# Optimization experiments

Measured on AMD Instinct MI355X. Metric: run time of the kernel, lower is better.

The kernel has to match this reference:

```python
import jax, jax.numpy as jnp
import numpy as np

P = 2          # patch size
DEPTH = 3
NHEAD = 8
DROP_RATIO = 0.15
LN_EPS = 1e-5


def _ln(x, g, b):
    m = jnp.mean(x, axis=-1, keepdims=True)
    v = jnp.mean((x - m) ** 2, axis=-1, keepdims=True)
    return (x - m) * jax.lax.rsqrt(v + LN_EPS) * g + b


def setup_inputs() -> dict:
    key = jax.random.key(0)
    ks = jax.random.split(key, 16)
    B, C, HW, D, L = 4, 3, 96, 256, DEPTH
    N = (HW // P) ** 2
    s = 0.02
    return {
        "x": jax.random.normal(ks[0], (B, C, HW, HW), jnp.float32),
        "patch_w": jax.random.normal(ks[1], (D, C, P, P), jnp.float32) * s,
        "patch_b": jnp.zeros((D,), jnp.float32),
        "pos": jax.random.normal(ks[2], (1, N, D), jnp.float32) * s,
        "imp_w1": jax.random.normal(ks[3], (D, 256), jnp.float32) * s,
        "imp_b1": jnp.zeros((256,), jnp.float32),
        "imp_w2": jax.random.normal(ks[4], (256, 1), jnp.float32) * s,
        "imp_b2": jnp.zeros((1,), jnp.float32),
        "ln1_g": jnp.ones((L, D), jnp.float32),
        "ln1_b": jnp.zeros((L, D), jnp.float32),
        "qkv_w": jax.random.normal(ks[5], (L, D, 3 * D), jnp.float32) * s,
        "qkv_b": jnp.zeros((L, 3 * D), jnp.float32),
        "proj_w": jax.random.normal(ks[6], (L, D, D), jnp.float32) * s,
        "proj_b": jnp.zeros((L, D), jnp.float32),
        "ln2_g": jnp.ones((L, D), jnp.float32),
        "ln2_b": jnp.zeros((L, D), jnp.float32),
        "mlp_w1": jax.random.normal(ks[7], (L, D, 4 * D), jnp.float32) * s,
        "mlp_b1": jnp.zeros((L, 4 * D), jnp.float32),
        "mlp_w2": jax.random.normal(ks[8], (L, 4 * D, D), jnp.float32) * s,
        "mlp_b2": jnp.zeros((L, D), jnp.float32),
        "out_g": jnp.ones((D,), jnp.float32),
        "out_b": jnp.zeros((D,), jnp.float32),
    }


def reference(x, patch_w, patch_b, pos, imp_w1, imp_b1, imp_w2, imp_b2,
              ln1_g, ln1_b, qkv_w, qkv_b, proj_w, proj_b,
              ln2_g, ln2_b, mlp_w1, mlp_b1, mlp_w2, mlp_b2, out_g, out_b):
    B, C, H, W = x.shape
    D = patch_w.shape[0]
    Hc, Wc = H // P, W // P
    # Patch embed: conv(k=stride=P) == blocked einsum  -> (B, N, D)
    xr = x.reshape(B, C, Hc, P, Wc, P)
    tokens = jnp.einsum('bchpwq,dcpq->bhwd', xr, patch_w).reshape(B, Hc * Wc, D) + patch_b
    tokens = tokens + pos
    B, N, _ = tokens.shape

    # Importance scores -> bottom-k keys masked (Eq.8-10)
    h = jax.nn.relu(tokens @ imp_w1 + imp_b1)
    scores = jax.nn.sigmoid((h @ imp_w2 + imp_b2)[..., 0])  # (B, N)
    k = int(DROP_RATIO * N)
    _, idx = jax.lax.top_k(-scores, k)                      # k smallest scores
    md = jnp.zeros((B, N), bool).at[jnp.arange(B)[:, None], idx].set(True)

    dk = D // NHEAD
    scale = 1.0 / np.sqrt(dk)
    for l in range(DEPTH):
        hln = _ln(tokens, ln1_g[l], ln1_b[l])
        qkv = hln @ qkv_w[l] + qkv_b[l]
        q, kk, v = jnp.split(qkv, 3, axis=-1)
        q = q.reshape(B, N, NHEAD, dk).transpose(0, 2, 1, 3)
        kk = kk.reshape(B, N, NHEAD, dk).transpose(0, 2, 1, 3)
        v = v.reshape(B, N, NHEAD, dk).transpose(0, 2, 1, 3)
        logits = jnp.einsum('bhnd,bhmd->bhnm', q, kk) * scale
        logits = jnp.where(md[:, None, None, :], -jnp.inf, logits)
        attn = jax.nn.softmax(logits, axis=-1)
        out = jnp.einsum('bhnm,bhmd->bhnd', attn, v)
        out = out.transpose(0, 2, 1, 3).reshape(B, N, D)
        tokens = tokens + (out @ proj_w[l] + proj_b[l])
        h2 = _ln(tokens, ln2_g[l], ln2_b[l])
        tokens = tokens + (jax.nn.gelu(h2 @ mlp_w1[l] + mlp_b1[l], approximate=False) @ mlp_w2[l] + mlp_b2[l])

    tokens = _ln(tokens, out_g, out_b)
    return tokens.mean(axis=1)  # (B, D)
```

## Files before the change

### kernel.cpp

```cpp
#include <hip/hip_runtime.h>
#include <hip/hip_bf16.h>
#include <math.h>

#define BATCH 4
#define NTOK  2304
#define DIM   256
#define NHEADS 8
#define HCDIM 48
#define KSEL  345
#define NKEEP 1959
#define NKC   1984
#define KT    31
#define KREM  39
#define LN_EPS 1e-5f

typedef unsigned short u16;
typedef __attribute__((ext_vector_type(8))) short bf16x8;
typedef __attribute__((ext_vector_type(4))) float f32x4;

__device__ __forceinline__ u16 f2bf(float x) {
  union { float f; unsigned u; } v; v.f = x;
  return (u16)((v.u + 0x7FFFu + ((v.u >> 16) & 1u)) >> 16);
}

__device__ __forceinline__ void gload_lds16(const u16* g, u16* l) {
  __builtin_amdgcn_global_load_lds((const __attribute__((address_space(1))) void*)g,
                                   (__attribute__((address_space(3))) void*)l, 16, 0, 0);
}

__global__ __launch_bounds__(256) void k_patch_embed(
    const float* __restrict__ x, const float* __restrict__ pw,
    const float* __restrict__ pb, const float* __restrict__ pos,
    float* __restrict__ tokens) {
  int blk = blockIdx.x;
  int b = blk / NTOK, n = blk % NTOK;
  int hc = n / HCDIM, wc = n % HCDIM;
  __shared__ float xs[12];
  int t = threadIdx.x;
  if (t < 12) {
    int c = t >> 2, p = (t >> 1) & 1, q = t & 1;
    xs[t] = x[((b * 3 + c) * 96 + (hc * 2 + p)) * 96 + (wc * 2 + q)];
  }
  __syncthreads();
  float acc = pb[t];
#pragma unroll
  for (int i = 0; i < 12; ++i) acc += xs[i] * pw[t * 12 + i];
  tokens[(size_t)(b * NTOK + n) * DIM + t] = acc + pos[n * DIM + t];
}

__global__ __launch_bounds__(256) void k_importance(
    const float* __restrict__ tokens, const float* __restrict__ w1,
    const float* __restrict__ b1, const float* __restrict__ w2,
    const float* __restrict__ b2, float* __restrict__ scores) {
  __shared__ float ts[16 * 256];
  __shared__ float hw[16 * 256];
  int base = blockIdx.x * 16;
  int t = threadIdx.x;
  for (int i = t; i < 16 * 256; i += 256) ts[i] = tokens[(size_t)base * 256 + i];
  __syncthreads();
  float acc[16];
#pragma unroll
  for (int r = 0; r < 16; ++r) acc[r] = b1[t];
  for (int i = 0; i < 256; ++i) {
    float w = w1[i * 256 + t];
#pragma unroll
    for (int r = 0; r < 16; ++r) acc[r] += ts[r * 256 + i] * w;
  }
  float w2v = w2[t];
#pragma unroll
  for (int r = 0; r < 16; ++r) hw[r * 256 + t] = fmaxf(acc[r], 0.f) * w2v;
  __syncthreads();
  if (t < 16) {
    float s = b2[0];
    for (int i = 0; i < 256; ++i) s += hw[t * 256 + i];
    scores[base + t] = 1.f / (1.f + expf(-s));
  }
}

__global__ __launch_bounds__(256) void k_select(const float* __restrict__ scores,
                                                int* __restrict__ cmap,
                                                u16* __restrict__ kvc) {
  int b = blockIdx.x, t = threadIdx.x;
  __shared__ unsigned sb[NTOK];
  __shared__ int cnt;
  __shared__ int pfl[256], pfe[256];
  __shared__ int remS;
  for (int i = t; i < NTOK; i += 256) sb[i] = __float_as_uint(scores[b * NTOK + i]);
  __syncthreads();
  unsigned prefix = 0;
  int r = KSEL;
  for (int bit = 31; bit >= 0; --bit) {
    if (t == 0) cnt = 0;
    __syncthreads();
    unsigned bmask = 1u << bit;
    unsigned hmask = (bit == 31) ? 0u : ~((bmask << 1) - 1u);
    int local = 0;
    for (int i = t; i < NTOK; i += 256)
      if ((sb[i] & hmask) == prefix && !(sb[i] & bmask)) local++;
    if (local) atomicAdd(&cnt, local);
    __syncthreads();
    int c0 = cnt;
    if (r > c0) { r -= c0; prefix |= bmask; }
    __syncthreads();
  }
  unsigned v = prefix;
  int cl = 0, ce = 0;
  int j0 = t * 9;
  for (int j = j0; j < j0 + 9; ++j) { cl += (sb[j] < v); ce += (sb[j] == v); }
  pfl[t] = cl; pfe[t] = ce;
  __syncthreads();
  if (t == 0) {
    int pl = 0, pe = 0;
    for (int i = 0; i < 256; ++i) {
      int a = pfl[i], e = pfe[i];
      pfl[i] = pl; pfe[i] = pe;
      pl += a; pe += e;
    }
    remS = KSEL - pl;
  }
  __syncthreads();
  int pl = pfl[t], pe = pfe[t], rem = remS;
  for (int j = j0; j < j0 + 9; ++j) {
    bool less = sb[j] < v, eq = sb[j] == v;
    bool drop = less || (eq && pe < rem);
    int dropped_before = pl + (pe < rem ? pe : rem);
    cmap[b * NTOK + j] = drop ? -1 : (j - dropped_before);
    pl += less; pe += eq;
  }
  for (int i = t; i < (NKC - NKEEP) * 512; i += 256)
    kvc[((size_t)b * NKC + NKEEP) * 512 + i] = 0;
}

__global__ __launch_bounds__(256) void k_ln4bf(
    const float* __restrict__ in, u16* __restrict__ out,
    const float* __restrict__ g, const float* __restrict__ bta) {
  int w = threadIdx.x >> 6, l = threadIdx.x & 63;
  size_t row = (size_t)blockIdx.x * 4 + w;
  float4 v = *(const float4*)(in + row * DIM + l * 4);
  float s = v.x + v.y + v.z + v.w;
  float ss = v.x * v.x + v.y * v.y + v.z * v.z + v.w * v.w;
#pragma unroll
  for (int o = 1; o < 64; o <<= 1) { s += __shfl_xor(s, o); ss += __shfl_xor(ss, o); }
  float m = s * (1.f / DIM);
  float inv = rsqrtf(ss * (1.f / DIM) - m * m + LN_EPS);
  float4 gv = *(const float4*)(g + l * 4);
  float4 bv = *(const float4*)(bta + l * 4);
  union { ushort4 u4; __hip_bfloat162 h2[2]; } o4;
  o4.h2[0] = __float22bfloat162_rn(make_float2((v.x - m) * inv * gv.x + bv.x,
                                               (v.y - m) * inv * gv.y + bv.y));
  o4.h2[1] = __float22bfloat162_rn(make_float2((v.z - m) * inv * gv.z + bv.z,
                                               (v.w - m) * inv * gv.w + bv.w));
  *(ushort4*)(out + row * DIM + l * 4) = o4.u4;
}

__global__ __launch_bounds__(256) void k_lnmean(
    const float* __restrict__ in, const float* __restrict__ g,
    const float* __restrict__ bta, float* __restrict__ part) {
  int chunk = blockIdx.x, b = blockIdx.y;
  int w = threadIdx.x >> 6, l = threadIdx.x & 63;
  float4 gv = *(const float4*)(g + l * 4);
  float4 bv = *(const float4*)(bta + l * 4);
  float4 acc = make_float4(0.f, 0.f, 0.f, 0.f);
  for (int i = 0; i < 16; ++i) {
    size_t row = (size_t)b * NTOK + chunk * 64 + w * 16 + i;
    float4 v = *(const float4*)(in + row * DIM + l * 4);
    float s = v.x + v.y + v.z + v.w;
    float ss = v.x * v.x + v.y * v.y + v.z * v.z + v.w * v.w;
#pragma unroll
    for (int o = 1; o < 64; o <<= 1) { s += __shfl_xor(s, o); ss += __shfl_xor(ss, o); }
    float m = s * (1.f / DIM);
    float inv = rsqrtf(ss * (1.f / DIM) - m * m + LN_EPS);
    acc.x += (v.x - m) * inv * gv.x + bv.x;
    acc.y += (v.y - m) * inv * gv.y + bv.y;
    acc.z += (v.z - m) * inv * gv.z + bv.z;
    acc.w += (v.w - m) * inv * gv.w + bv.w;
  }
  __shared__ float4 red[4][64];
  red[w][l] = acc;
  __syncthreads();
  if (w == 0) {
    float4 a0 = red[0][l], a1 = red[1][l], a2 = red[2][l], a3 = red[3][l];
    float4 tot = make_float4(a0.x + a1.x + a2.x + a3.x, a0.y + a1.y + a2.y + a3.y,
                             a0.z + a1.z + a2.z + a3.z, a0.w + a1.w + a2.w + a3.w);
    *(float4*)(part + ((size_t)b * 36 + chunk) * DIM + l * 4) = tot;
  }
}

__global__ __launch_bounds__(256) void k_mean_final(const float* __restrict__ part,
                                                    float* __restrict__ out) {
  int b = blockIdx.x, d = threadIdx.x;
  float s = 0.f;
  for (int c = 0; c < 36; ++c) s += part[(size_t)(b * 36 + c) * DIM + d];
  out[b * DIM + d] = s * (1.0f / NTOK);
}

__global__ __launch_bounds__(256) void k_wtrans_all(
    const float* __restrict__ qkv_w, const float* __restrict__ proj_w,
    const float* __restrict__ mlp_w1, const float* __restrict__ mlp_w2,
    u16* __restrict__ wq, u16* __restrict__ wp,
    u16* __restrict__ w1, u16* __restrict__ w2) {
  int id = blockIdx.x;
  const float* W; u16* WT; int K, N, m;
  if (id < 576)       { m = id;        K = 256;  N = 768;  W = qkv_w;  WT = wq; }
  else if (id < 768)  { m = id - 576;  K = 256;  N = 256;  W = proj_w; WT = wp; }
  else if (id < 1536) { m = id - 768;  K = 256;  N = 1024; W = mlp_w1; WT = w1; }
  else                { m = id - 1536; K = 1024; N = 256;  W = mlp_w2; WT = w2; }
  int ntiles = N / 32, tilesPerLayer = ntiles * (K / 32);
  int layer = m / tilesPerLayer, tid = m % tilesPerLayer;
  int nb = (tid % ntiles) * 32, kb = (tid / ntiles) * 32;
  const float* Wl = W + (size_t)layer * K * N;
  u16* WTl = WT + (size_t)layer * K * N;
  __shared__ float tile[32][33];
  int tx = threadIdx.x & 31, ty = threadIdx.x >> 5;
  for (int i = 0; i < 32; i += 8) tile[ty + i][tx] = Wl[(size_t)(kb + ty + i) * N + nb + tx];
  __syncthreads();
  for (int i = 0; i < 32; i += 8)
    WTl[(size_t)(nb + ty + i) * K + kb + tx] = f2bf(tile[tx][ty + i]);
}

__global__ __launch_bounds__(256) void k_gemm_bf16(
    const u16* __restrict__ A, const u16* __restrict__ BT,
    const float* __restrict__ bias, u16* __restrict__ outb,
    int K, int N, int act) {
  __shared__ __align__(16) u16 As[2][128 * 32];
  __shared__ __align__(16) u16 Bs[2][128 * 32];
  int t = threadIdx.x;
  int m0 = blockIdx.y * 128, n0 = blockIdx.x * 128;
  int w = t >> 6, l = t & 63, lr = l & 15, qd = l >> 4;
  int wm = (w >> 1) * 64, wn = (w & 1) * 64;
  const u16* gA = A + (size_t)(m0 + w * 16 + (l >> 2)) * K + (l & 3) * 8;
  const u16* gA2 = gA + (size_t)64 * K;
  const u16* gB = BT + (size_t)(n0 + w * 16 + (l >> 2)) * K + (l & 3) * 8;
  const u16* gB2 = gB + (size_t)64 * K;
  f32x4 acc[4][4];
#pragma unroll
  for (int i = 0; i < 4; ++i)
#pragma unroll
    for (int j = 0; j < 4; ++j)
#pragma unroll
      for (int r = 0; r < 4; ++r) acc[i][j][r] = 0.f;
  gload_lds16(gA, As[0] + w * 512);
  gload_lds16(gA2, As[0] + 2048 + w * 512);
  gload_lds16(gB, Bs[0] + w * 512);
  gload_lds16(gB2, Bs[0] + 2048 + w * 512);
  int nchunks = K >> 5;
  for (int c = 0; c < nchunks; ++c) {
    int buf = c & 1;
    __syncthreads();
    if (c + 1 < nchunks) {
      int k0 = (c + 1) << 5;
      gload_lds16(gA + k0, As[buf ^ 1] + w * 512);
      gload_lds16(gA2 + k0, As[buf ^ 1] + 2048 + w * 512);
      gload_lds16(gB + k0, Bs[buf ^ 1] + w * 512);
      gload_lds16(gB2 + k0, Bs[buf ^ 1] + 2048 + w * 512);
    }
    bf16x8 af[4], bfr[4];
#pragma unroll
    for (int mt = 0; mt < 4; ++mt)
      af[mt] = *(const bf16x8*)(As[buf] + (wm + mt * 16 + lr) * 32 + qd * 8);
#pragma unroll
    for (int nt = 0; nt < 4; ++nt)
      bfr[nt] = *(const bf16x8*)(Bs[buf] + (wn + nt * 16 + lr) * 32 + qd * 8);
#pragma unroll
    for (int mt = 0; mt < 4; ++mt)
#pragma unroll
      for (int nt = 0; nt < 4; ++nt)
        acc[mt][nt] = __builtin_amdgcn_mfma_f32_16x16x32_bf16(af[mt], bfr[nt],
                                                              acc[mt][nt], 0, 0, 0);
  }
#pragma unroll
  for (int mt = 0; mt < 4; ++mt) {
#pragma unroll
    for (int nt = 0; nt < 4; ++nt) {
#pragma unroll
      for (int r = 0; r < 4; ++r) {
        size_t m = (size_t)m0 + wm + mt * 16 + qd * 4 + r;
        int c = n0 + wn + nt * 16 + lr;
        float val = acc[mt][nt][r] + bias[c];
        if (act) val = 0.5f * val * (1.f + erff(val * 0.70710678118654752f));
        outb[m * N + c] = f2bf(val);
      }
    }
  }
}

__global__ __launch_bounds__(256) void k_gemm_qkv(
    const u16* __restrict__ A, const u16* __restrict__ BT,
    const float* __restrict__ bias, const int* __restrict__ cmap,
    u16* __restrict__ Qb, u16* __restrict__ KVc) {
  const int K = 256, N = 768;
  __shared__ __align__(16) u16 As[2][128 * 32];
  __shared__ __align__(16) u16 Bs[2][128 * 32];
  int t = threadIdx.x;
  int m0 = blockIdx.y * 128, n0 = blockIdx.x * 128;
  int w = t >> 6, l = t & 63, lr = l & 15, qd = l >> 4;
  int wm = (w >> 1) * 64, wn = (w & 1) * 64;
  const u16* gA = A + (size_t)(m0 + w * 16 + (l >> 2)) * K + (l & 3) * 8;
  const u16* gA2 = gA + (size_t)64 * K;
  const u16* gB = BT + (size_t)(n0 + w * 16 + (l >> 2)) * K + (l & 3) * 8;
  const u16* gB2 = gB + (size_t)64 * K;
  f32x4 acc[4][4];
#pragma unroll
  for (int i = 0; i < 4; ++i)
#pragma unroll
    for (int j = 0; j < 4; ++j)
#pragma unroll
      for (int r = 0; r < 4; ++r) acc[i][j][r] = 0.f;
  gload_lds16(gA, As[0] + w * 512);
  gload_lds16(gA2, As[0] + 2048 + w * 512);
  gload_lds16(gB, Bs[0] + w * 512);
  gload_lds16(gB2, Bs[0] + 2048 + w * 512);
  for (int c = 0; c < 8; ++c) {
    int buf = c & 1;
    __syncthreads();
    if (c + 1 < 8) {
      int k0 = (c + 1) << 5;
      gload_lds16(gA + k0, As[buf ^ 1] + w * 512);
      gload_lds16(gA2 + k0, As[buf ^ 1] + 2048 + w * 512);
      gload_lds16(gB + k0, Bs[buf ^ 1] + w * 512);
      gload_lds16(gB2 + k0, Bs[buf ^ 1] + 2048 + w * 512);
    }
    bf16x8 af[4], bfr[4];
#pragma unroll
    for (int mt = 0; mt < 4; ++mt)
      af[mt] = *(const bf16x8*)(As[buf] + (wm + mt * 16 + lr) * 32 + qd * 8);
#pragma unroll
    for (int nt = 0; nt < 4; ++nt)
      bfr[nt] = *(const bf16x8*)(Bs[buf] + (wn + nt * 16 + lr) * 32 + qd * 8);
#pragma unroll
    for (int mt = 0; mt < 4; ++mt)
#pragma unroll
      for (int nt = 0; nt < 4; ++nt)
        acc[mt][nt] = __builtin_amdgcn_mfma_f32_16x16x32_bf16(af[mt], bfr[nt],
                                                              acc[mt][nt], 0, 0, 0);
  }
  bool isQ = (n0 + wn) < 256;
#pragma unroll
  for (int mt = 0; mt < 4; ++mt) {
#pragma unroll
    for (int r = 0; r < 4; ++r) {
      int m = m0 + wm + mt * 16 + qd * 4 + r;
      int cpos = isQ ? 0 : cmap[m];
      int b = m / NTOK;
#pragma unroll
      for (int nt = 0; nt < 4; ++nt) {
        int c = n0 + wn + nt * 16 + lr;
        float val = acc[mt][nt][r] + bias[c];
        if (isQ) {
          Qb[(size_t)m * 256 + c] = f2bf(val * 0.17677669529663687f);
        } else if (cpos >= 0) {
          KVc[((size_t)b * NKC + cpos) * 512 + (c - 256)] = f2bf(val);
        }
      }
    }
  }
}

__global__ __launch_bounds__(256) void k_gemm_n64(
    const u16* __restrict__ A, const u16* __restrict__ BT,
    const float* __restrict__ bias, const float* __restrict__ res,
    float* __restrict__ outf, int K, int N) {
  __shared__ __align__(16) u16 As[2][128 * 32];
  __shared__ __align__(16) u16 Bs[2][64 * 32];
  int t = threadIdx.x;
  int m0 = blockIdx.y * 128, n0 = blockIdx.x * 64;
  int w = t >> 6, l = t & 63, lr = l & 15, qd = l >> 4;
  int wm = (w >> 1) * 64, wn = (w & 1) * 32;
  const u16* gA = A + (size_t)(m0 + w * 16 + (l >> 2)) * K + (l & 3) * 8;
  const u16* gA2 = gA + (size_t)64 * K;
  const u16* gB = BT + (size_t)(n0 + w * 16 + (l >> 2)) * K + (l & 3) * 8;
  f32x4 acc[4][2];
#pragma unroll
  for (int i = 0; i < 4; ++i)
#pragma unroll
    for (int j = 0; j < 2; ++j)
#pragma unroll
      for (int r = 0; r < 4; ++r) acc[i][j][r] = 0.f;
  gload_lds16(gA, As[0] + w * 512);
  gload_lds16(gA2, As[0] + 2048 + w * 512);
  gload_lds16(gB, Bs[0] + w * 512);
  int nchunks = K >> 5;
  for (int c = 0; c < nchunks; ++c) {
    int buf = c & 1;
    __syncthreads();
    if (c + 1 < nchunks) {
      int k0 = (c + 1) << 5;
      gload_lds16(gA + k0, As[buf ^ 1] + w * 512);
      gload_lds16(gA2 + k0, As[buf ^ 1] + 2048 + w * 512);
      gload_lds16(gB + k0, Bs[buf ^ 1] + w * 512);
    }
    bf16x8 af[4], bfr[2];
#pragma unroll
    for (int mt = 0; mt < 4; ++mt)
      af[mt] = *(const bf16x8*)(As[buf] + (wm + mt * 16 + lr) * 32 + qd * 8);
#pragma unroll
    for (int nt = 0; nt < 2; ++nt)
      bfr[nt] = *(const bf16x8*)(Bs[buf] + (wn + nt * 16 + lr) * 32 + qd * 8);
#pragma unroll
    for (int mt = 0; mt < 4; ++mt)
#pragma unroll
      for (int nt = 0; nt < 2; ++nt)
        acc[mt][nt] = __builtin_amdgcn_mfma_f32_16x16x32_bf16(af[mt], bfr[nt],
                                                              acc[mt][nt], 0, 0, 0);
  }
#pragma unroll
  for (int mt = 0; mt < 4; ++mt) {
#pragma unroll
    for (int nt = 0; nt < 2; ++nt) {
#pragma unroll
      for (int r = 0; r < 4; ++r) {
        size_t m = (size_t)m0 + wm + mt * 16 + qd * 4 + r;
        int c = n0 + wn + nt * 16 + lr;
        outf[m * N + c] = acc[mt][nt][r] + bias[c] + res[m * N + c];
      }
    }
  }
}

__global__ __launch_bounds__(256) void k_attn4(
    const u16* __restrict__ Qb, const u16* __restrict__ KVc,
    u16* __restrict__ outb) {
  int qt = blockIdx.x, h = blockIdx.y, b = blockIdx.z;
  int t = threadIdx.x, w = t >> 6, l = t & 63, lr = l & 15, qd = l >> 4;
  __shared__ __align__(16) u16 Ks[2][64 * 32];
  __shared__ __align__(16) u16 Vt[2][32][80];
  __shared__ __align__(16) u16 Pq[4][32][80];
  const short ONE = (short)0x3F80;
  int q0 = qt * 128 + w * 32;
  const u16* kvb = KVc + (size_t)b * NKC * 512;
  bf16x8 qf[2];
  qf[0] = *(const bf16x8*)(Qb + ((size_t)(b * NTOK) + q0 + lr) * 256 + h * 32 + qd * 8);
  qf[1] = *(const bf16x8*)(Qb + ((size_t)(b * NTOK) + q0 + 16 + lr) * 256 + h * 32 + qd * 8);
  const u16* gK = kvb + (size_t)(t >> 2) * 512 + h * 32 + (t & 3) * 8;
  const u16* gV = kvb + (size_t)l * 512 + 256 + h * 32 + w * 8;
  gload_lds16(gK, &Ks[0][w * 512]);
  bf16x8 vr = *(const bf16x8*)(gV);
  f32x4 oa[2][2];
  f32x4 lacc[2];
#pragma unroll
  for (int r = 0; r < 4; ++r) {
    oa[0][0][r] = 0.f; oa[0][1][r] = 0.f; oa[1][0][r] = 0.f; oa[1][1][r] = 0.f;
    lacc[0][r] = 0.f; lacc[1][r] = 0.f;
  }
  bf16x8 ones;
#pragma unroll
  for (int j = 0; j < 8; ++j) ones[j] = ONE;
  for (int kt = 0; kt < KT; ++kt) {
    int buf = kt & 1;
#pragma unroll
    for (int j = 0; j < 8; ++j) Vt[buf][w * 8 + j][l] = (u16)vr[j];
    __syncthreads();
    if (kt + 1 < KT) {
      size_t off = (size_t)(kt + 1) * 64 * 512;
      gload_lds16(gK + off, &Ks[buf ^ 1][w * 512]);
      vr = *(const bf16x8*)(gV + off);
    }
    bf16x8 kf[4];
#pragma unroll
    for (int nt = 0; nt < 4; ++nt)
      kf[nt] = *(const bf16x8*)(&Ks[buf][(nt * 16 + lr) * 32 + qd * 8]);
#pragma unroll
    for (int qh = 0; qh < 2; ++qh) {
      f32x4 p4[4];
#pragma unroll
      for (int nt = 0; nt < 4; ++nt) {
        f32x4 z; z[0] = 0.f; z[1] = 0.f; z[2] = 0.f; z[3] = 0.f;
        p4[nt] = __builtin_amdgcn_mfma_f32_16x16x32_bf16(kf[nt], qf[qh], z, 0, 0, 0);
      }
#pragma unroll
      for (int nt = 0; nt < 4; ++nt)
#pragma unroll
        for (int r = 0; r < 4; ++r) p4[nt][r] = __expf(p4[nt][r]);
#pragma unroll
      for (int nt = 0; nt < 4; ++nt) {
        union { ushort4 u4; __hip_bfloat162 h2[2]; } pu;
        pu.h2[0] = __float22bfloat162_rn(make_float2(p4[nt][0], p4[nt][1]));
        pu.h2[1] = __float22bfloat162_rn(make_float2(p4[nt][2], p4[nt][3]));
        *(ushort4*)(&Pq[w][qh * 16 + lr][nt * 16 + qd * 4]) = pu.u4;
      }
    }
    bf16x8 of1 = ones;
    if (kt == KT - 1) {
#pragma unroll
      for (int j = 0; j < 8; ++j) of1[j] = (32 + qd * 8 + j < KREM) ? ONE : (short)0;
    }
#pragma unroll
    for (int qh = 0; qh < 2; ++qh) {
#pragma unroll
      for (int kh = 0; kh < 2; ++kh) {
        bf16x8 pf = *(const bf16x8*)(&Pq[w][qh * 16 + lr][kh * 32 + qd * 8]);
#pragma unroll
        for (int dh = 0; dh < 2; ++dh) {
          bf16x8 vf = *(const bf16x8*)(&Vt[buf][dh * 16 + lr][kh * 32 + qd * 8]);
          oa[qh][dh] = __builtin_amdgcn_mfma_f32_16x16x32_bf16(pf, vf, oa[qh][dh], 0, 0, 0);
        }
        lacc[qh] = __builtin_amdgcn_mfma_f32_16x16x32_bf16(
            pf, kh ? of1 : ones, lacc[qh], 0, 0, 0);
      }
    }
  }
#pragma unroll
  for (int qh = 0; qh < 2; ++qh) {
#pragma unroll
    for (int r = 0; r < 4; ++r) {
      float inv = 1.f / lacc[qh][r];
      size_t row = (size_t)b * NTOK + q0 + qh * 16 + qd * 4 + r;
      outb[row * 256 + h * 32 + lr] = f2bf(oa[qh][0][r] * inv);
      outb[row * 256 + h * 32 + 16 + lr] = f2bf(oa[qh][1][r] * inv);
    }
  }
}

extern "C" void kernel_launch(void* const* d_in, const int* in_sizes, int n_in,
                              void* d_out, int out_size, void* d_ws, size_t ws_size,
                              hipStream_t stream) {
  (void)in_sizes; (void)n_in; (void)out_size;
  const float* x       = (const float*)d_in[0];
  const float* patch_w = (const float*)d_in[1];
  const float* patch_b = (const float*)d_in[2];
  const float* pos     = (const float*)d_in[3];
  const float* imp_w1  = (const float*)d_in[4];
  const float* imp_b1  = (const float*)d_in[5];
  const float* imp_w2  = (const float*)d_in[6];
  const float* imp_b2  = (const float*)d_in[7];
  const float* ln1_g   = (const float*)d_in[8];
  const float* ln1_b   = (const float*)d_in[9];
  const float* qkv_w   = (const float*)d_in[10];
  const float* qkv_b   = (const float*)d_in[11];
  const float* proj_w  = (const float*)d_in[12];
  const float* proj_b  = (const float*)d_in[13];
  const float* ln2_g   = (const float*)d_in[14];
  const float* ln2_b   = (const float*)d_in[15];
  const float* mlp_w1  = (const float*)d_in[16];
  const float* mlp_b1  = (const float*)d_in[17];
  const float* mlp_w2  = (const float*)d_in[18];
  const float* mlp_b2  = (const float*)d_in[19];
  const float* out_g   = (const float*)d_in[20];
  const float* out_b   = (const float*)d_in[21];
  float* out = (float*)d_out;

  const int M = BATCH * NTOK;
  const size_t TOK = (size_t)M * DIM;

  char* p = (char*)d_ws;
  float* tokens = (float*)p;       p += TOK * 4;
  float* scoresp = (float*)p;      p += (size_t)M * 4;
  int* cmap = (int*)p;             p += (size_t)M * 4;
  u16* act_bf = (u16*)p;           p += TOK * 2;
  u16* Qb = (u16*)p;               p += TOK * 2;
  u16* kvc = (u16*)p;              p += (size_t)BATCH * NKC * 512 * 2;
  u16* big_bf = (u16*)p;           p += (size_t)M * 1024 * 2;
  u16* wq_t = (u16*)p;             p += (size_t)3 * 768 * 256 * 2;
  u16* wp_t = (u16*)p;             p += (size_t)3 * 256 * 256 * 2;
  u16* w1_t = (u16*)p;             p += (size_t)3 * 1024 * 256 * 2;
  u16* w2_t = (u16*)p;             p += (size_t)3 * 256 * 1024 * 2;
  float* partials = (float*)act_bf;
  if (ws_size < (size_t)(p - (char*)d_ws)) return;

  k_wtrans_all<<<dim3(2304), 256, 0, stream>>>(qkv_w, proj_w, mlp_w1, mlp_w2,
                                               wq_t, wp_t, w1_t, w2_t);
  k_patch_embed<<<dim3(M), 256, 0, stream>>>(x, patch_w, patch_b, pos, tokens);
  k_importance<<<dim3(M / 16), 256, 0, stream>>>(tokens, imp_w1, imp_b1, imp_w2, imp_b2, scoresp);
  k_select<<<dim3(BATCH), 256, 0, stream>>>(scoresp, cmap, kvc);

  for (int l = 0; l < 3; ++l) {
    k_ln4bf<<<dim3(M / 4), 256, 0, stream>>>(tokens, act_bf, ln1_g + l * DIM, ln1_b + l * DIM);
    k_gemm_qkv<<<dim3(6, 72), 256, 0, stream>>>(
        act_bf, wq_t + (size_t)l * 768 * 256, qkv_b + l * 768, cmap, Qb, kvc);
    k_attn4<<<dim3(18, NHEADS, BATCH), 256, 0, stream>>>(Qb, kvc, act_bf);
    k_gemm_n64<<<dim3(4, 72), 256, 0, stream>>>(
        act_bf, wp_t + (size_t)l * 256 * 256, proj_b + l * DIM, tokens, tokens, 256, 256);
    k_ln4bf<<<dim3(M / 4), 256, 0, stream>>>(tokens, act_bf, ln2_g + l * DIM, ln2_b + l * DIM);
    k_gemm_bf16<<<dim3(8, 72), 256, 0, stream>>>(
        act_bf, w1_t + (size_t)l * 1024 * 256, mlp_b1 + l * 1024, big_bf, 256, 1024, 1);
    k_gemm_n64<<<dim3(4, 72), 256, 0, stream>>>(
        big_bf, w2_t + (size_t)l * 256 * 1024, mlp_b2 + l * DIM, tokens, tokens, 1024, 256);
  }
  k_lnmean<<<dim3(36, BATCH), 256, 0, stream>>>(tokens, out_g, out_b, partials);
  k_mean_final<<<dim3(BATCH), 256, 0, stream>>>(partials, out);
}
```

Baseline: 613.6 us.

## Swizzle LDS tiles, shrink attention and N64 GEMM tiles, use exp2 softmax

Applies an XOR swizzle to the LDS column offsets in all GEMM kernels and the attention K tile, aiming to cut LDS bank conflicts on the bf16x8 fragment reads. Halves the M tile of the N=256 GEMM (64x64 tiles, twice as many blocks) and halves the query rows per wave in attention (16 instead of 32, twice as many blocks), trading per-block reuse for more parallelism across CUs. Folds log2(e) into the Q scale so the softmax can use a native exp2 instead of __expf. The smaller attention tiles reload K/V more often, and the smaller GEMM tiles reload more weight data.

```diff
diff --git a/kernel.cpp b/kernel.cpp
--- a/kernel.cpp
+++ b/kernel.cpp
@@ -13,6 +13,7 @@
 #define KT    31
 #define KREM  39
 #define LN_EPS 1e-5f
+#define QSCALE 0.25508688726880056f
 
 typedef unsigned short u16;
 typedef __attribute__((ext_vector_type(8))) short bf16x8;
@@ -228,9 +229,11 @@
   int m0 = blockIdx.y * 128, n0 = blockIdx.x * 128;
   int w = t >> 6, l = t & 63, lr = l & 15, qd = l >> 4;
   int wm = (w >> 1) * 64, wn = (w & 1) * 64;
-  const u16* gA = A + (size_t)(m0 + w * 16 + (l >> 2)) * K + (l & 3) * 8;
+  int sc = ((t & 3) ^ ((t >> 4) & 3)) * 8;
+  int rc = (qd ^ ((lr >> 2) & 3)) * 8;
+  const u16* gA = A + (size_t)(m0 + w * 16 + (l >> 2)) * K + sc;
   const u16* gA2 = gA + (size_t)64 * K;
-  const u16* gB = BT + (size_t)(n0 + w * 16 + (l >> 2)) * K + (l & 3) * 8;
+  const u16* gB = BT + (size_t)(n0 + w * 16 + (l >> 2)) * K + sc;
   const u16* gB2 = gB + (size_t)64 * K;
   f32x4 acc[4][4];
 #pragma unroll
@@ -257,10 +260,10 @@
     bf16x8 af[4], bfr[4];
 #pragma unroll
     for (int mt = 0; mt < 4; ++mt)
-      af[mt] = *(const bf16x8*)(As[buf] + (wm + mt * 16 + lr) * 32 + qd * 8);
+      af[mt] = *(const bf16x8*)(As[buf] + (wm + mt * 16 + lr) * 32 + rc);
 #pragma unroll
     for (int nt = 0; nt < 4; ++nt)
-      bfr[nt] = *(const bf16x8*)(Bs[buf] + (wn + nt * 16 + lr) * 32 + qd * 8);
+      bfr[nt] = *(const bf16x8*)(Bs[buf] + (wn + nt * 16 + lr) * 32 + rc);
 #pragma unroll
     for (int mt = 0; mt < 4; ++mt)
 #pragma unroll
@@ -295,9 +298,11 @@
   int m0 = blockIdx.y * 128, n0 = blockIdx.x * 128;
   int w = t >> 6, l = t & 63, lr = l & 15, qd = l >> 4;
   int wm = (w >> 1) * 64, wn = (w & 1) * 64;
-  const u16* gA = A + (size_t)(m0 + w * 16 + (l >> 2)) * K + (l & 3) * 8;
+  int sc = ((t & 3) ^ ((t >> 4) & 3)) * 8;
+  int rc = (qd ^ ((lr >> 2) & 3)) * 8;
+  const u16* gA = A + (size_t)(m0 + w * 16 + (l >> 2)) * K + sc;
   const u16* gA2 = gA + (size_t)64 * K;
-  const u16* gB = BT + (size_t)(n0 + w * 16 + (l >> 2)) * K + (l & 3) * 8;
+  const u16* gB = BT + (size_t)(n0 + w * 16 + (l >> 2)) * K + sc;
   const u16* gB2 = gB + (size_t)64 * K;
   f32x4 acc[4][4];
 #pragma unroll
@@ -323,10 +328,10 @@
     bf16x8 af[4], bfr[4];
 #pragma unroll
     for (int mt = 0; mt < 4; ++mt)
-      af[mt] = *(const bf16x8*)(As[buf] + (wm + mt * 16 + lr) * 32 + qd * 8);
+      af[mt] = *(const bf16x8*)(As[buf] + (wm + mt * 16 + lr) * 32 + rc);
 #pragma unroll
     for (int nt = 0; nt < 4; ++nt)
-      bfr[nt] = *(const bf16x8*)(Bs[buf] + (wn + nt * 16 + lr) * 32 + qd * 8);
+      bfr[nt] = *(const bf16x8*)(Bs[buf] + (wn + nt * 16 + lr) * 32 + rc);
 #pragma unroll
     for (int mt = 0; mt < 4; ++mt)
 #pragma unroll
@@ -347,7 +352,7 @@
         int c = n0 + wn + nt * 16 + lr;
         float val = acc[mt][nt][r] + bias[c];
         if (isQ) {
-          Qb[(size_t)m * 256 + c] = f2bf(val * 0.17677669529663687f);
+          Qb[(size_t)m * 256 + c] = f2bf(val * QSCALE);
         } else if (cpos >= 0) {
           KVc[((size_t)b * NKC + cpos) * 512 + (c - 256)] = f2bf(val);
         }
@@ -360,24 +365,24 @@
     const u16* __restrict__ A, const u16* __restrict__ BT,
     const float* __restrict__ bias, const float* __restrict__ res,
     float* __restrict__ outf, int K, int N) {
-  __shared__ __align__(16) u16 As[2][128 * 32];
+  __shared__ __align__(16) u16 As[2][64 * 32];
   __shared__ __align__(16) u16 Bs[2][64 * 32];
   int t = threadIdx.x;
-  int m0 = blockIdx.y * 128, n0 = blockIdx.x * 64;
+  int m0 = blockIdx.y * 64, n0 = blockIdx.x * 64;
   int w = t >> 6, l = t & 63, lr = l & 15, qd = l >> 4;
-  int wm = (w >> 1) * 64, wn = (w & 1) * 32;
-  const u16* gA = A + (size_t)(m0 + w * 16 + (l >> 2)) * K + (l & 3) * 8;
-  const u16* gA2 = gA + (size_t)64 * K;
-  const u16* gB = BT + (size_t)(n0 + w * 16 + (l >> 2)) * K + (l & 3) * 8;
-  f32x4 acc[4][2];
-#pragma unroll
-  for (int i = 0; i < 4; ++i)
+  int wm = (w >> 1) * 32, wn = (w & 1) * 32;
+  int sc = ((t & 3) ^ ((t >> 4) & 3)) * 8;
+  int rc = (qd ^ ((lr >> 2) & 3)) * 8;
+  const u16* gA = A + (size_t)(m0 + w * 16 + (l >> 2)) * K + sc;
+  const u16* gB = BT + (size_t)(n0 + w * 16 + (l >> 2)) * K + sc;
+  f32x4 acc[2][2];
+#pragma unroll
+  for (int i = 0; i < 2; ++i)
 #pragma unroll
     for (int j = 0; j < 2; ++j)
 #pragma unroll
       for (int r = 0; r < 4; ++r) acc[i][j][r] = 0.f;
   gload_lds16(gA, As[0] + w * 512);
-  gload_lds16(gA2, As[0] + 2048 + w * 512);
   gload_lds16(gB, Bs[0] + w * 512);
   int nchunks = K >> 5;
   for (int c = 0; c < nchunks; ++c) {
@@ -386,25 +391,24 @@
     if (c + 1 < nchunks) {
       int k0 = (c + 1) << 5;
       gload_lds16(gA + k0, As[buf ^ 1] + w * 512);
-      gload_lds16(gA2 + k0, As[buf ^ 1] + 2048 + w * 512);
       gload_lds16(gB + k0, Bs[buf ^ 1] + w * 512);
     }
-    bf16x8 af[4], bfr[2];
-#pragma unroll
-    for (int mt = 0; mt < 4; ++mt)
-      af[mt] = *(const bf16x8*)(As[buf] + (wm + mt * 16 + lr) * 32 + qd * 8);
+    bf16x8 af[2], bfr[2];
+#pragma unroll
+    for (int mt = 0; mt < 2; ++mt)
+      af[mt] = *(const bf16x8*)(As[buf] + (wm + mt * 16 + lr) * 32 + rc);
 #pragma unroll
     for (int nt = 0; nt < 2; ++nt)
-      bfr[nt] = *(const bf16x8*)(Bs[buf] + (wn + nt * 16 + lr) * 32 + qd * 8);
-#pragma unroll
-    for (int mt = 0; mt < 4; ++mt)
+      bfr[nt] = *(const bf16x8*)(Bs[buf] + (wn + nt * 16 + lr) * 32 + rc);
+#pragma unroll
+    for (int mt = 0; mt < 2; ++mt)
 #pragma unroll
       for (int nt = 0; nt < 2; ++nt)
         acc[mt][nt] = __builtin_amdgcn_mfma_f32_16x16x32_bf16(af[mt], bfr[nt],
                                                               acc[mt][nt], 0, 0, 0);
   }
 #pragma unroll
-  for (int mt = 0; mt < 4; ++mt) {
+  for (int mt = 0; mt < 2; ++mt) {
 #pragma unroll
     for (int nt = 0; nt < 2; ++nt) {
 #pragma unroll
@@ -417,31 +421,27 @@
   }
 }
 
-__global__ __launch_bounds__(256) void k_attn4(
+__global__ __launch_bounds__(256) void k_attn6(
     const u16* __restrict__ Qb, const u16* __restrict__ KVc,
     u16* __restrict__ outb) {
   int qt = blockIdx.x, h = blockIdx.y, b = blockIdx.z;
   int t = threadIdx.x, w = t >> 6, l = t & 63, lr = l & 15, qd = l >> 4;
   __shared__ __align__(16) u16 Ks[2][64 * 32];
-  __shared__ __align__(16) u16 Vt[2][32][80];
-  __shared__ __align__(16) u16 Pq[4][32][80];
+  __shared__ __align__(16) u16 Vt[2][32][72];
+  __shared__ __align__(16) u16 Pq[4][16][72];
   const short ONE = (short)0x3F80;
-  int q0 = qt * 128 + w * 32;
+  int q0 = qt * 64 + w * 16;
+  bf16x8 qf = *(const bf16x8*)(Qb + ((size_t)(b * NTOK) + q0 + lr) * 256 + h * 32 + qd * 8);
   const u16* kvb = KVc + (size_t)b * NKC * 512;
-  bf16x8 qf[2];
-  qf[0] = *(const bf16x8*)(Qb + ((size_t)(b * NTOK) + q0 + lr) * 256 + h * 32 + qd * 8);
-  qf[1] = *(const bf16x8*)(Qb + ((size_t)(b * NTOK) + q0 + 16 + lr) * 256 + h * 32 + qd * 8);
-  const u16* gK = kvb + (size_t)(t >> 2) * 512 + h * 32 + (t & 3) * 8;
+  const u16* gK = kvb + (size_t)(t >> 2) * 512 + h * 32 + ((t & 3) ^ ((t >> 4) & 3)) * 8;
   const u16* gV = kvb + (size_t)l * 512 + 256 + h * 32 + w * 8;
+  int rc = (qd ^ ((lr >> 2) & 3)) * 8;
   gload_lds16(gK, &Ks[0][w * 512]);
   bf16x8 vr = *(const bf16x8*)(gV);
-  f32x4 oa[2][2];
-  f32x4 lacc[2];
-#pragma unroll
-  for (int r = 0; r < 4; ++r) {
-    oa[0][0][r] = 0.f; oa[0][1][r] = 0.f; oa[1][0][r] = 0.f; oa[1][1][r] = 0.f;
-    lacc[0][r] = 0.f; lacc[1][r] = 0.f;
-  }
+  f32x4 oa[2];
+  f32x4 lacc;
+#pragma unroll
+  for (int r = 0; r < 4; ++r) { oa[0][r] = 0.f; oa[1][r] = 0.f; lacc[r] = 0.f; }
   bf16x8 ones;
 #pragma unroll
   for (int j = 0; j < 8; ++j) ones[j] = ONE;
@@ -455,29 +455,23 @@
       gload_lds16(gK + off, &Ks[buf ^ 1][w * 512]);
       vr = *(const bf16x8*)(gV + off);
     }
-    bf16x8 kf[4];
+    f32x4 p4[4];
+#pragma unroll
+    for (int nt = 0; nt < 4; ++nt) {
+      bf16x8 kf = *(const bf16x8*)(&Ks[buf][(nt * 16 + lr) * 32 + rc]);
+      f32x4 z; z[0] = 0.f; z[1] = 0.f; z[2] = 0.f; z[3] = 0.f;
+      p4[nt] = __builtin_amdgcn_mfma_f32_16x16x32_bf16(kf, qf, z, 0, 0, 0);
+    }
 #pragma unroll
     for (int nt = 0; nt < 4; ++nt)
-      kf[nt] = *(const bf16x8*)(&Ks[buf][(nt * 16 + lr) * 32 + qd * 8]);
-#pragma unroll
-    for (int qh = 0; qh < 2; ++qh) {
-      f32x4 p4[4];
-#pragma unroll
-      for (int nt = 0; nt < 4; ++nt) {
-        f32x4 z; z[0] = 0.f; z[1] = 0.f; z[2] = 0.f; z[3] = 0.f;
-        p4[nt] = __builtin_amdgcn_mfma_f32_16x16x32_bf16(kf[nt], qf[qh], z, 0, 0, 0);
-      }
-#pragma unroll
-      for (int nt = 0; nt < 4; ++nt)
-#pragma unroll
-        for (int r = 0; r < 4; ++r) p4[nt][r] = __expf(p4[nt][r]);
-#pragma unroll
-      for (int nt = 0; nt < 4; ++nt) {
-        union { ushort4 u4; __hip_bfloat162 h2[2]; } pu;
-        pu.h2[0] = __float22bfloat162_rn(make_float2(p4[nt][0], p4[nt][1]));
-        pu.h2[1] = __float22bfloat162_rn(make_float2(p4[nt][2], p4[nt][3]));
-        *(ushort4*)(&Pq[w][qh * 16 + lr][nt * 16 + qd * 4]) = pu.u4;
-      }
+#pragma unroll
+      for (int r = 0; r < 4; ++r) p4[nt][r] = __builtin_amdgcn_exp2f(p4[nt][r]);
+#pragma unroll
+    for (int nt = 0; nt < 4; ++nt) {
+      union { ushort4 u4; __hip_bfloat162 h2[2]; } pu;
+      pu.h2[0] = __float22bfloat162_rn(make_float2(p4[nt][0], p4[nt][1]));
+      pu.h2[1] = __float22bfloat162_rn(make_float2(p4[nt][2], p4[nt][3]));
+      *(ushort4*)(&Pq[w][lr][nt * 16 + qd * 4]) = pu.u4;
     }
     bf16x8 of1 = ones;
     if (kt == KT - 1) {
@@ -485,29 +479,22 @@
       for (int j = 0; j < 8; ++j) of1[j] = (32 + qd * 8 + j < KREM) ? ONE : (short)0;
     }
 #pragma unroll
-    for (int qh = 0; qh < 2; ++qh) {
-#pragma unroll
-      for (int kh = 0; kh < 2; ++kh) {
-        bf16x8 pf = *(const bf16x8*)(&Pq[w][qh * 16 + lr][kh * 32 + qd * 8]);
-#pragma unroll
-        for (int dh = 0; dh < 2; ++dh) {
-          bf16x8 vf = *(const bf16x8*)(&Vt[buf][dh * 16 + lr][kh * 32 + qd * 8]);
-          oa[qh][dh] = __builtin_amdgcn_mfma_f32_16x16x32_bf16(pf, vf, oa[qh][dh], 0, 0, 0);
-        }
-        lacc[qh] = __builtin_amdgcn_mfma_f32_16x16x32_bf16(
-            pf, kh ? of1 : ones, lacc[qh], 0, 0, 0);
+    for (int kh = 0; kh < 2; ++kh) {
+      bf16x8 pf = *(const bf16x8*)(&Pq[w][lr][kh * 32 + qd * 8]);
+#pragma unroll
+      for (int dh = 0; dh < 2; ++dh) {
+        bf16x8 vf = *(const bf16x8*)(&Vt[buf][dh * 16 + lr][kh * 32 + qd * 8]);
+        oa[dh] = __builtin_amdgcn_mfma_f32_16x16x32_bf16(pf, vf, oa[dh], 0, 0, 0);
       }
-    }
-  }
-#pragma unroll
-  for (int qh = 0; qh < 2; ++qh) {
-#pragma unroll
-    for (int r = 0; r < 4; ++r) {
-      float inv = 1.f / lacc[qh][r];
-      size_t row = (size_t)b * NTOK + q0 + qh * 16 + qd * 4 + r;
-      outb[row * 256 + h * 32 + lr] = f2bf(oa[qh][0][r] * inv);
-      outb[row * 256 + h * 32 + 16 + lr] = f2bf(oa[qh][1][r] * inv);
-    }
+      lacc = __builtin_amdgcn_mfma_f32_16x16x32_bf16(pf, kh ? of1 : ones, lacc, 0, 0, 0);
+    }
+  }
+#pragma unroll
+  for (int r = 0; r < 4; ++r) {
+    float inv = 1.f / lacc[r];
+    size_t row = (size_t)b * NTOK + q0 + qd * 4 + r;
+    outb[row * 256 + h * 32 + lr] = f2bf(oa[0][r] * inv);
+    outb[row * 256 + h * 32 + 16 + lr] = f2bf(oa[1][r] * inv);
   }
 }
 
@@ -567,13 +554,13 @@
     k_ln4bf<<<dim3(M / 4), 256, 0, stream>>>(tokens, act_bf, ln1_g + l * DIM, ln1_b + l * DIM);
     k_gemm_qkv<<<dim3(6, 72), 256, 0, stream>>>(
         act_bf, wq_t + (size_t)l * 768 * 256, qkv_b + l * 768, cmap, Qb, kvc);
-    k_attn4<<<dim3(18, NHEADS, BATCH), 256, 0, stream>>>(Qb, kvc, act_bf);
-    k_gemm_n64<<<dim3(4, 72), 256, 0, stream>>>(
+    k_attn6<<<dim3(36, NHEADS, BATCH), 256, 0, stream>>>(Qb, kvc, act_bf);
+    k_gemm_n64<<<dim3(4, 144), 256, 0, stream>>>(
         act_bf, wp_t + (size_t)l * 256 * 256, proj_b + l * DIM, tokens, tokens, 256, 256);
     k_ln4bf<<<dim3(M / 4), 256, 0, stream>>>(tokens, act_bf, ln2_g + l * DIM, ln2_b + l * DIM);
     k_gemm_bf16<<<dim3(8, 72), 256, 0, stream>>>(
         act_bf, w1_t + (size_t)l * 1024 * 256, mlp_b1 + l * 1024, big_bf, 256, 1024, 1);
-    k_gemm_n64<<<dim3(4, 72), 256, 0, stream>>>(
+    k_gemm_n64<<<dim3(4, 144), 256, 0, stream>>>(
         big_bf, w2_t + (size_t)l * 256 * 1024, mlp_b2 + l * DIM, tokens, tokens, 1024, 256);
   }
   k_lnmean<<<dim3(36, BATCH), 256, 0, stream>>>(tokens, out_g, out_b, partials);
```

Result: faster. 571.3 us (-6.9%).
